# Kernel optimization log

Hardware: AMD Instinct MI355X
Metric: run time of the kernel (lower is better)

Reference implementation:

```python
import jax, jax.numpy as jnp
import numpy as np

EPS = 1e-8  # torch.cosine_similarity default eps


def setup_inputs() -> dict:
    key = jax.random.key(0)
    k1, k2 = jax.random.split(key)
    infeatures, capacity = 4096, 65536
    x = jax.random.normal(k1, (infeatures,), dtype=jnp.float32)
    # nn.Parameter(torch.rand(infeatures)) -> uniform [0,1)
    memory = jax.random.uniform(k2, (capacity, infeatures), dtype=jnp.float32)
    return {"x": x, "memory": memory}


def reference(x, memory):
    # cosine_similarity(x, memory[i], dim=0) for every slot i, fused:
    # dots:  [capacity] = memory @ x
    dots = memory @ x
    mem_norm = jnp.sqrt(jnp.sum(memory * memory, axis=1))  # [capacity]
    x_norm = jnp.sqrt(jnp.sum(x * x))                      # scalar
    denom = jnp.maximum(mem_norm * x_norm, EPS)
    return dots / denom
```

## Files before the change

kernel.cpp:

```cpp
#include <hip/hip_runtime.h>
#include <math.h>

#define INFEAT 4096
#define CAPACITY 65536
#define EPS 1e-8f

__global__ void xnorm_kernel(const float* __restrict__ x, float* __restrict__ ws) {
    const int tid = threadIdx.x;
    float s = 0.f;
    #pragma unroll
    for (int i = tid; i < INFEAT; i += 256) {
        float v = x[i];
        s += v * v;
    }
    #pragma unroll
    for (int off = 32; off > 0; off >>= 1) s += __shfl_down(s, off);
    __shared__ float partial[4];
    const int wid  = tid >> 6;
    const int lane = tid & 63;
    if (lane == 0) partial[wid] = s;
    __syncthreads();
    if (tid == 0) {
        float t = partial[0] + partial[1] + partial[2] + partial[3];
        ws[0] = sqrtf(t);
    }
}

__global__ __launch_bounds__(256) void cosine_kernel(const float* __restrict__ x,
                                                     const float* __restrict__ memory,
                                                     const float* __restrict__ ws,
                                                     float* __restrict__ out) {
    const int lane = threadIdx.x & 63;
    const int wid  = threadIdx.x >> 6;
    const int wave = blockIdx.x * 4 + wid;
    const int nwaves = gridDim.x * 4;
    const float xn = ws[0];

    const float4* x4 = reinterpret_cast<const float4*>(x);
    float4 xr[16];
    #pragma unroll
    for (int k = 0; k < 16; ++k) xr[k] = x4[lane + k * 64];

    for (int row = wave; row < CAPACITY; row += nwaves) {
        const float4* m4 =
            reinterpret_cast<const float4*>(memory + (size_t)row * INFEAT);
        float dot0 = 0.f, dot1 = 0.f, ss0 = 0.f, ss1 = 0.f;
        #pragma unroll
        for (int k = 0; k < 16; k += 2) {
            float4 a = m4[lane + k * 64];
            float4 b = m4[lane + (k + 1) * 64];
            dot0 = fmaf(a.x, xr[k].x, dot0);
            dot0 = fmaf(a.y, xr[k].y, dot0);
            dot0 = fmaf(a.z, xr[k].z, dot0);
            dot0 = fmaf(a.w, xr[k].w, dot0);
            ss0  = fmaf(a.x, a.x, ss0);
            ss0  = fmaf(a.y, a.y, ss0);
            ss0  = fmaf(a.z, a.z, ss0);
            ss0  = fmaf(a.w, a.w, ss0);
            dot1 = fmaf(b.x, xr[k + 1].x, dot1);
            dot1 = fmaf(b.y, xr[k + 1].y, dot1);
            dot1 = fmaf(b.z, xr[k + 1].z, dot1);
            dot1 = fmaf(b.w, xr[k + 1].w, dot1);
            ss1  = fmaf(b.x, b.x, ss1);
            ss1  = fmaf(b.y, b.y, ss1);
            ss1  = fmaf(b.z, b.z, ss1);
            ss1  = fmaf(b.w, b.w, ss1);
        }
        float dot = dot0 + dot1;
        float ss  = ss0 + ss1;
        #pragma unroll
        for (int off = 32; off > 0; off >>= 1) {
            dot += __shfl_down(dot, off);
            ss  += __shfl_down(ss, off);
        }
        if (lane == 0) {
            float denom = fmaxf(sqrtf(ss) * xn, EPS);
            out[row] = dot / denom;
        }
    }
}

extern "C" void kernel_launch(void* const* d_in, const int* in_sizes, int n_in,
                              void* d_out, int out_size, void* d_ws, size_t ws_size,
                              hipStream_t stream) {
    const float* x      = (const float*)d_in[0];
    const float* memory = (const float*)d_in[1];
    float* out = (float*)d_out;
    float* ws  = (float*)d_ws;

    xnorm_kernel<<<1, 256, 0, stream>>>(x, ws);
    cosine_kernel<<<2048, 256, 0, stream>>>(x, memory, ws, out);
}
```

Before: 191.1 us.

## Fuse x-norm into cosine kernel, stage x in LDS, use nontemporal loads

Removes the separate x-norm kernel launch: each block now loads x into shared memory and reduces its norm itself. Each wave handles a contiguous group of 8 rows instead of a grid-stride loop. The x vector is read from LDS instead of being held in 64 registers, which frees VGPRs for higher occupancy (launch bounds 256,8). Memory rows use nontemporal loads and the output uses a nontemporal store to avoid polluting cache. The cost is redundant x loading and norm work in every block, plus LDS traffic inside the inner loop.

```diff
diff --git a/kernel.cpp b/kernel.cpp
--- a/kernel.cpp
+++ b/kernel.cpp
@@ -4,63 +4,65 @@
 #define INFEAT 4096
 #define CAPACITY 65536
 #define EPS 1e-8f
+#define NBLOCKS 2048
+#define ROWS_PER_WAVE 8
 
-__global__ void xnorm_kernel(const float* __restrict__ x, float* __restrict__ ws) {
-    const int tid = threadIdx.x;
-    float s = 0.f;
+typedef float f32x4 __attribute__((ext_vector_type(4)));
+
+__global__ __launch_bounds__(256, 8) void cosine_kernel(const float* __restrict__ x,
+                                                        const float* __restrict__ memory,
+                                                        float* __restrict__ out) {
+    __shared__ float sx[INFEAT];
+    __shared__ float partial[4];
+
+    const int tid  = threadIdx.x;
+    const int lane = tid & 63;
+    const int wid  = tid >> 6;
+
+    const f32x4* x4  = reinterpret_cast<const f32x4*>(x);
+    f32x4*       sx4 = reinterpret_cast<f32x4*>(sx);
+    float ssx = 0.f;
     #pragma unroll
-    for (int i = tid; i < INFEAT; i += 256) {
-        float v = x[i];
-        s += v * v;
+    for (int k = 0; k < 4; ++k) {
+        f32x4 v = x4[tid + k * 256];
+        sx4[tid + k * 256] = v;
+        ssx = fmaf(v.x, v.x, ssx);
+        ssx = fmaf(v.y, v.y, ssx);
+        ssx = fmaf(v.z, v.z, ssx);
+        ssx = fmaf(v.w, v.w, ssx);
     }
     #pragma unroll
-    for (int off = 32; off > 0; off >>= 1) s += __shfl_down(s, off);
-    __shared__ float partial[4];
-    const int wid  = tid >> 6;
-    const int lane = tid & 63;
-    if (lane == 0) partial[wid] = s;
+    for (int off = 32; off > 0; off >>= 1) ssx += __shfl_down(ssx, off);
+    if (lane == 0) partial[wid] = ssx;
     __syncthreads();
-    if (tid == 0) {
-        float t = partial[0] + partial[1] + partial[2] + partial[3];
-        ws[0] = sqrtf(t);
-    }
-}
+    const float xn = sqrtf(partial[0] + partial[1] + partial[2] + partial[3]);
 
-__global__ __launch_bounds__(256) void cosine_kernel(const float* __restrict__ x,
-                                                     const float* __restrict__ memory,
-                                                     const float* __restrict__ ws,
-                                                     float* __restrict__ out) {
-    const int lane = threadIdx.x & 63;
-    const int wid  = threadIdx.x >> 6;
-    const int wave = blockIdx.x * 4 + wid;
-    const int nwaves = gridDim.x * 4;
-    const float xn = ws[0];
+    const int  wave = blockIdx.x * 4 + wid;
+    const long row0 = (long)wave * ROWS_PER_WAVE;
 
-    const float4* x4 = reinterpret_cast<const float4*>(x);
-    float4 xr[16];
-    #pragma unroll
-    for (int k = 0; k < 16; ++k) xr[k] = x4[lane + k * 64];
-
-    for (int row = wave; row < CAPACITY; row += nwaves) {
-        const float4* m4 =
-            reinterpret_cast<const float4*>(memory + (size_t)row * INFEAT);
+    for (int r = 0; r < ROWS_PER_WAVE; ++r) {
+        const long row = row0 + r;
+        const f32x4* m4 =
+            reinterpret_cast<const f32x4*>(memory + row * INFEAT);
         float dot0 = 0.f, dot1 = 0.f, ss0 = 0.f, ss1 = 0.f;
         #pragma unroll
         for (int k = 0; k < 16; k += 2) {
-            float4 a = m4[lane + k * 64];
-            float4 b = m4[lane + (k + 1) * 64];
-            dot0 = fmaf(a.x, xr[k].x, dot0);
-            dot0 = fmaf(a.y, xr[k].y, dot0);
-            dot0 = fmaf(a.z, xr[k].z, dot0);
-            dot0 = fmaf(a.w, xr[k].w, dot0);
+            f32x4 a  = __builtin_nontemporal_load(&m4[lane + k * 64]);
+            f32x4 b  = __builtin_nontemporal_load(&m4[lane + (k + 1) * 64]);
+            f32x4 xa = sx4[lane + k * 64];
+            f32x4 xb = sx4[lane + (k + 1) * 64];
+            dot0 = fmaf(a.x, xa.x, dot0);
+            dot0 = fmaf(a.y, xa.y, dot0);
+            dot0 = fmaf(a.z, xa.z, dot0);
+            dot0 = fmaf(a.w, xa.w, dot0);
             ss0  = fmaf(a.x, a.x, ss0);
             ss0  = fmaf(a.y, a.y, ss0);
             ss0  = fmaf(a.z, a.z, ss0);
             ss0  = fmaf(a.w, a.w, ss0);
-            dot1 = fmaf(b.x, xr[k + 1].x, dot1);
-            dot1 = fmaf(b.y, xr[k + 1].y, dot1);
-            dot1 = fmaf(b.z, xr[k + 1].z, dot1);
-            dot1 = fmaf(b.w, xr[k + 1].w, dot1);
+            dot1 = fmaf(b.x, xb.x, dot1);
+            dot1 = fmaf(b.y, xb.y, dot1);
+            dot1 = fmaf(b.z, xb.z, dot1);
+            dot1 = fmaf(b.w, xb.w, dot1);
             ss1  = fmaf(b.x, b.x, ss1);
             ss1  = fmaf(b.y, b.y, ss1);
             ss1  = fmaf(b.z, b.z, ss1);
@@ -75,7 +77,7 @@
         }
         if (lane == 0) {
             float denom = fmaxf(sqrtf(ss) * xn, EPS);
-            out[row] = dot / denom;
+            __builtin_nontemporal_store(dot / denom, &out[row]);
         }
     }
 }
@@ -86,8 +88,6 @@
     const float* x      = (const float*)d_in[0];
     const float* memory = (const float*)d_in[1];
     float* out = (float*)d_out;
-    float* ws  = (float*)d_ws;
 
-    xnorm_kernel<<<1, 256, 0, stream>>>(x, ws);
-    cosine_kernel<<<2048, 256, 0, stream>>>(x, memory, ws, out);
+    cosine_kernel<<<NBLOCKS, 256, 0, stream>>>(x, memory, out);
 }
```

New measurement: 250.7 us. 31.2% more time.
